# Kernel tuning notes

Measured on AMD Instinct MI355X. Metric: run time of the kernel, lower is better.

## Reference

```python
import jax, jax.numpy as jnp
import numpy as np

B, S, D, H = 4, 2048, 1024, 16
DH = D // H


def setup_inputs() -> dict:
    key = jax.random.key(0)
    ks = jax.random.split(key, 12)
    std = 0.02
    return {
        "inputs": jax.random.normal(ks[0], (B, S, D), jnp.float32),
        "pre_block": jax.random.normal(ks[1], (B, S, D), jnp.float32),
        "ln_gamma": jnp.ones((D,), jnp.float32),
        "ln_beta": jnp.zeros((D,), jnp.float32),
        "Wq": jax.random.normal(ks[2], (D, D), jnp.float32) * std,
        "bq": jnp.zeros((D,), jnp.float32),
        "Wk": jax.random.normal(ks[3], (D, D), jnp.float32) * std,
        "bk": jnp.zeros((D,), jnp.float32),
        "Wv": jax.random.normal(ks[4], (D, D), jnp.float32) * std,
        "bv": jnp.zeros((D,), jnp.float32),
        "Wpos": jax.random.normal(ks[5], (D, D), jnp.float32) * std,
        "u_bias": jax.random.normal(ks[6], (H, DH), jnp.float32) * std,
        "v_bias": jax.random.normal(ks[7], (H, DH), jnp.float32) * std,
        "Wo": jax.random.normal(ks[8], (D, D), jnp.float32) * std,
        "bo": jnp.zeros((D,), jnp.float32),
    }


def _sinusoidal_pe(seq_len, d_model, dtype):
    pos = jnp.arange(seq_len, dtype=dtype)[:, None]                 # [S,1]
    i = jnp.arange(0, d_model, 2, dtype=dtype)
    div = jnp.exp(-(jnp.log(jnp.asarray(10000.0, dtype)) * i / d_model))  # [D/2]
    ang = pos * div                                                  # [S,D/2]
    pe = jnp.zeros((seq_len, d_model), dtype)
    pe = pe.at[:, 0::2].set(jnp.sin(ang)).at[:, 1::2].set(jnp.cos(ang))
    return pe


def _rel_shift(pos_score):
    # Transformer-XL style relative shift: pos_score [B,H,S,S]
    b, h, s1, s2 = pos_score.shape
    pad = jnp.zeros((b, h, s1, 1), pos_score.dtype)
    padded = jnp.concatenate([pad, pos_score], axis=-1)              # [B,H,S,S+1]
    padded = padded.reshape(b, h, s2 + 1, s1)
    return padded[:, :, 1:].reshape(b, h, s1, s2)


def _layer_norm(x, gamma, beta, eps=1e-5):
    mu = jnp.mean(x, axis=-1, keepdims=True)
    var = jnp.mean(jnp.square(x - mu), axis=-1, keepdims=True)
    return (x - mu) * jax.lax.rsqrt(var + eps) * gamma + beta


def reference(inputs, pre_block, ln_gamma, ln_beta, Wq, bq, Wk, bk, Wv, bv,
              Wpos, u_bias, v_bias, Wo, bo):
    b, s, d = inputs.shape
    h = u_bias.shape[0]
    dh = d // h

    pe = _sinusoidal_pe(s, d, inputs.dtype)                          # [S,D]
    x = _layer_norm(inputs, ln_gamma, ln_beta)

    q = (x @ Wq + bq).reshape(b, s, h, dh)
    k = (x @ Wk + bk).reshape(b, s, h, dh)
    v = (pre_block @ Wv + bv).reshape(b, s, h, dh)
    p = (pe @ Wpos).reshape(s, h, dh)                                # shared across batch

    content = jnp.einsum('bshd,bthd->bhst', q + u_bias, k)           # [B,H,S,S]
    pos_score = jnp.einsum('bshd,thd->bhst', q + v_bias, p)          # [B,H,S,S]
    pos_score = _rel_shift(pos_score)

    score = (content + pos_score) / jnp.sqrt(jnp.asarray(d, inputs.dtype))
    attn = jax.nn.softmax(score, axis=-1)
    ctx = jnp.einsum('bhst,bthd->bshd', attn, v).reshape(b, s, d)
    return ctx @ Wo + bo
```

## Files before the change

kernel.cpp:

```cpp
#include <hip/hip_runtime.h>
#include <hip/hip_bf16.h>
#include <cmath>

#define B_ 4
#define S_ 2048
#define D_ 1024
#define H_ 16
#define DH_ 64

typedef __attribute__((ext_vector_type(8))) short short8;
typedef __attribute__((ext_vector_type(4))) float f32x4;
#define MFMA_BF16(a, b, c) __builtin_amdgcn_mfma_f32_16x16x32_bf16(a, b, c, 0, 0, 0)

static __device__ __forceinline__ float b2f(unsigned short u) {
  union { unsigned int i; float f; } x; x.i = ((unsigned int)u) << 16; return x.f;
}
static __device__ __forceinline__ unsigned short f2b(float f) {
  union { float f; unsigned int i; } x; x.f = f;
  unsigned int r = x.i + 0x7FFFu + ((x.i >> 16) & 1u);
  return (unsigned short)(r >> 16);
}
static __device__ __forceinline__ unsigned int pk2(float a, float b) {
  __hip_bfloat162 h = __float22bfloat162_rn(make_float2(a, b));
  return *(unsigned int*)&h;
}
static __device__ __forceinline__ int mod96(int x) {
  int t = x >> 5;
  int q = (t * 43691) >> 17;
  int m3 = t - q * 3;
  return (x & 31) + (m3 << 5);
}
static __device__ __forceinline__ int clampS(int x) {
  return x < 0 ? 0 : (x > S_ - 1 ? S_ - 1 : x);
}
typedef __attribute__((address_space(3))) unsigned int lds_u32_t;
typedef __attribute__((address_space(1))) const unsigned int glb_u32_t;
static __device__ __forceinline__ void gload_lds16(const void* g, void* l) {
  __builtin_amdgcn_global_load_lds((glb_u32_t*)g, (lds_u32_t*)l, 16, 0, 0);
}

__global__ __launch_bounds__(256) void prep_kernel(
    const float* __restrict__ inputs, const float* __restrict__ gamma,
    const float* __restrict__ beta, unsigned short* __restrict__ xb,
    const float* __restrict__ pre, unsigned short* __restrict__ preb,
    const double* __restrict__ dt, unsigned short* __restrict__ pe,
    const float* __restrict__ Wq, unsigned short* __restrict__ wtq,
    const float* __restrict__ Wk, unsigned short* __restrict__ wtk,
    const float* __restrict__ Wv, unsigned short* __restrict__ wtv,
    const float* __restrict__ Wp, unsigned short* __restrict__ wtp,
    const float* __restrict__ Wo, unsigned short* __restrict__ wto) {
  __shared__ __align__(16) float shf[64 * 65];
  int bid = blockIdx.x;
  int tid = threadIdx.x;
  if (bid < 8192) {
    int row = bid;
    float4 val = ((const float4*)(inputs + (size_t)row * D_))[tid];
    float s = val.x + val.y + val.z + val.w;
    float sq = val.x * val.x + val.y * val.y + val.z * val.z + val.w * val.w;
#pragma unroll
    for (int o = 32; o > 0; o >>= 1) {
      s += __shfl_down(s, o);
      sq += __shfl_down(sq, o);
    }
    int wid = tid >> 6;
    if ((tid & 63) == 0) { shf[wid] = s; shf[4 + wid] = sq; }
    __syncthreads();
    if (tid == 0) {
      float ts = shf[0] + shf[1] + shf[2] + shf[3];
      float tq = shf[4] + shf[5] + shf[6] + shf[7];
      float mu = ts * (1.0f / D_);
      float var = tq * (1.0f / D_) - mu * mu;
      shf[8] = mu;
      shf[9] = rsqrtf(var + 1e-5f);
    }
    __syncthreads();
    float mu = shf[8], rs = shf[9];
    float4 g = ((const float4*)gamma)[tid];
    float4 be = ((const float4*)beta)[tid];
    ushort4 o;
    o.x = f2b((val.x - mu) * rs * g.x + be.x);
    o.y = f2b((val.y - mu) * rs * g.y + be.y);
    o.z = f2b((val.z - mu) * rs * g.z + be.z);
    o.w = f2b((val.w - mu) * rs * g.w + be.w);
    *(ushort4*)(xb + (size_t)row * D_ + tid * 4) = o;
    return;
  }
  bid -= 8192;
  if (bid < 8192) {
    size_t idx = (size_t)(bid * 256 + tid) * 4;
    float4 v = *(const float4*)(pre + idx);
    ushort4 o; o.x = f2b(v.x); o.y = f2b(v.y); o.z = f2b(v.z); o.w = f2b(v.w);
    *(ushort4*)(preb + idx) = o;
    return;
  }
  bid -= 8192;
  if (bid < 4096) {
    int idx = bid * 256 + tid;
    int t = idx >> 9;
    int i = idx & 511;
    double ang = (double)t * dt[i];
    double k = floor(ang * 0.15915494309189535);
    float red = (float)(ang - k * 6.283185307179586);
    ushort2 sc;
    sc.x = f2b(sinf(red));
    sc.y = f2b(cosf(red));
    *(ushort2*)(pe + (size_t)t * D_ + 2 * i) = sc;
    return;
  }
  bid -= 4096;
  const float* W; unsigned short* WT;
  switch (bid >> 8) {
    case 0: W = Wq; WT = wtq; break;
    case 1: W = Wk; WT = wtk; break;
    case 2: W = Wv; WT = wtv; break;
    case 3: W = Wp; WT = wtp; break;
    default: W = Wo; WT = wto; break;
  }
  int tile = bid & 255;
  int n0 = (tile & 15) * 64, k0 = (tile >> 4) * 64;
#pragma unroll
  for (int c = 0; c < 4; c++) {
    int idx = tid + c * 256;
    int r = idx >> 4;
    int ch = (idx & 15) * 4;
    float4 d = *(const float4*)(W + (size_t)(k0 + r) * D_ + n0 + ch);
    shf[r * 65 + ch] = d.x; shf[r * 65 + ch + 1] = d.y;
    shf[r * 65 + ch + 2] = d.z; shf[r * 65 + ch + 3] = d.w;
  }
  __syncthreads();
  {
    int n = tid >> 2;
    int ch = (tid & 3) * 16;
    unsigned short tmp[8];
#pragma unroll
    for (int half = 0; half < 2; half++) {
#pragma unroll
      for (int e = 0; e < 8; e++) tmp[e] = f2b(shf[(ch + half * 8 + e) * 65 + n]);
      *(short8*)(WT + (size_t)(n0 + n) * D_ + k0 + ch + half * 8) = *(short8*)tmp;
    }
  }
}

template <bool F32OUT>
__global__ __launch_bounds__(256) void gemm_bf16_t(const unsigned short* __restrict__ A,
                                                   const unsigned short* __restrict__ BT,
                                                   const float* __restrict__ bias,
                                                   void* __restrict__ Cv,
                                                   int M, int N, int K) {
  __shared__ __align__(16) unsigned short As[128 * 32];
  __shared__ __align__(16) unsigned short Bs[128 * 32];
  const int tid = threadIdx.x;
  const int wid = tid >> 6, lane = tid & 63, quad = lane >> 4, l15 = lane & 15;
  const int m0 = blockIdx.y * 128, n0 = blockIdx.x * 128;
  const int moff = (wid >> 1) * 64, noff = (wid & 1) * 64;
  f32x4 acc[4][4];
#pragma unroll
  for (int i = 0; i < 4; i++)
#pragma unroll
    for (int j = 0; j < 4; j++) acc[i][j] = (f32x4){0.f, 0.f, 0.f, 0.f};

  const int cb0 = wid * 64;
  const int c0 = cb0 + lane;
  const int r0 = c0 >> 2, ch0 = (c0 & 3) * 8;
  const int c1 = c0 + 256;
  const int r1 = c1 >> 2, ch1 = (c1 & 3) * 8;

  for (int k0 = 0; k0 < K; k0 += 32) {
    __syncthreads();
    gload_lds16(A + (size_t)(m0 + r0) * K + k0 + ch0, &As[cb0 * 8]);
    gload_lds16(BT + (size_t)(n0 + r0) * K + k0 + ch0, &Bs[cb0 * 8]);
    gload_lds16(A + (size_t)(m0 + r1) * K + k0 + ch1, &As[(cb0 + 256) * 8]);
    gload_lds16(BT + (size_t)(n0 + r1) * K + k0 + ch1, &Bs[(cb0 + 256) * 8]);
    __syncthreads();
    short8 af[4], bf[4];
#pragma unroll
    for (int i = 0; i < 4; i++)
      af[i] = *(const short8*)&As[(moff + i * 16 + l15) * 32 + quad * 8];
#pragma unroll
    for (int j = 0; j < 4; j++)
      bf[j] = *(const short8*)&Bs[(noff + j * 16 + l15) * 32 + quad * 8];
#pragma unroll
    for (int i = 0; i < 4; i++)
#pragma unroll
      for (int j = 0; j < 4; j++) acc[i][j] = MFMA_BF16(af[i], bf[j], acc[i][j]);
  }
#pragma unroll
  for (int i = 0; i < 4; i++) {
    int row = m0 + moff + i * 16 + quad * 4;
#pragma unroll
    for (int j = 0; j < 4; j++) {
      int col = n0 + noff + j * 16 + l15;
      float bb = bias ? bias[col] : 0.f;
#pragma unroll
      for (int g = 0; g < 4; g++) {
        if (F32OUT)
          ((float*)Cv)[(size_t)(row + g) * N + col] = acc[i][j][g] + bb;
        else
          ((unsigned short*)Cv)[(size_t)(row + g) * N + col] = f2b(acc[i][j][g] + bb);
      }
    }
  }
}

__global__ __launch_bounds__(256) void gemm_qk_bf16(const unsigned short* __restrict__ A,
                                                    const unsigned short* __restrict__ BT,
                                                    const float* __restrict__ bq,
                                                    const float* __restrict__ bk,
                                                    unsigned short* __restrict__ outQ,
                                                    unsigned short* __restrict__ outK) {
  const int K = D_;
  __shared__ __align__(16) unsigned short As[128 * 32];
  __shared__ __align__(16) unsigned short Bs[128 * 32];
  const int tid = threadIdx.x;
  const int wid = tid >> 6, lane = tid & 63, quad = lane >> 4, l15 = lane & 15;
  const int m0 = blockIdx.y * 128, n0 = blockIdx.x * 128;
  const int moff = (wid >> 1) * 64, noff = (wid & 1) * 64;
  f32x4 acc[4][4];
#pragma unroll
  for (int i = 0; i < 4; i++)
#pragma unroll
    for (int j = 0; j < 4; j++) acc[i][j] = (f32x4){0.f, 0.f, 0.f, 0.f};

  const int cb0 = wid * 64;
  const int c0 = cb0 + lane;
  const int r0 = c0 >> 2, ch0 = (c0 & 3) * 8;
  const int c1 = c0 + 256;
  const int r1 = c1 >> 2, ch1 = (c1 & 3) * 8;

  for (int k0 = 0; k0 < K; k0 += 32) {
    __syncthreads();
    gload_lds16(A + (size_t)(m0 + r0) * K + k0 + ch0, &As[cb0 * 8]);
    gload_lds16(BT + (size_t)(n0 + r0) * K + k0 + ch0, &Bs[cb0 * 8]);
    gload_lds16(A + (size_t)(m0 + r1) * K + k0 + ch1, &As[(cb0 + 256) * 8]);
    gload_lds16(BT + (size_t)(n0 + r1) * K + k0 + ch1, &Bs[(cb0 + 256) * 8]);
    __syncthreads();
    short8 af[4], bf[4];
#pragma unroll
    for (int i = 0; i < 4; i++)
      af[i] = *(const short8*)&As[(moff + i * 16 + l15) * 32 + quad * 8];
#pragma unroll
    for (int j = 0; j < 4; j++)
      bf[j] = *(const short8*)&Bs[(noff + j * 16 + l15) * 32 + quad * 8];
#pragma unroll
    for (int i = 0; i < 4; i++)
#pragma unroll
      for (int j = 0; j < 4; j++) acc[i][j] = MFMA_BF16(af[i], bf[j], acc[i][j]);
  }
  const float* bias = (n0 < D_) ? bq : bk;
  unsigned short* outp = (n0 < D_) ? outQ : outK;
  const int nn0 = n0 & (D_ - 1);
#pragma unroll
  for (int i = 0; i < 4; i++) {
    int row = m0 + moff + i * 16 + quad * 4;
#pragma unroll
    for (int j = 0; j < 4; j++) {
      int col = nn0 + noff + j * 16 + l15;
      float bb = bias[col];
#pragma unroll
      for (int g = 0; g < 4; g++)
        outp[(size_t)(row + g) * D_ + col] = f2b(acc[i][j][g] + bb);
    }
  }
}

__global__ __launch_bounds__(256) void post_kernel(const unsigned short* __restrict__ v,
                                                   unsigned short* __restrict__ vt) {
  __shared__ __align__(16) unsigned short t[64 * 72];
  int bid = blockIdx.x;
  int tid = threadIdx.x;
  int s0 = (bid & 31) * 64, h = (bid >> 5) & 15, b = bid >> 9;
#pragma unroll
  for (int c = 0; c < 2; c++) {
    int idx = tid + c * 256;
    int r = idx >> 3, ch = (idx & 7) * 8;
    short8 d = *(const short8*)(v + (((size_t)b * S_ + s0 + r) * H_ + h) * DH_ + ch);
    *(short8*)&t[r * 72 + ch] = d;
  }
  __syncthreads();
  int dh = tid >> 2, ch = tid & 3;
  unsigned short tmp[8];
#pragma unroll
  for (int half = 0; half < 2; half++) {
#pragma unroll
    for (int e = 0; e < 8; e++) tmp[e] = t[(ch * 16 + half * 8 + e) * 72 + dh];
    *(short8*)(vt + ((size_t)(b * H_ + h) * 64 + dh) * S_ + s0 + ch * 16 + half * 8) =
        *(short8*)tmp;
  }
}

__global__ __launch_bounds__(256) void attn_kernel(const unsigned short* __restrict__ q,
                                                   const unsigned short* __restrict__ kg,
                                                   const unsigned short* __restrict__ vtg,
                                                   const unsigned short* __restrict__ pg,
                                                   const float* __restrict__ ub,
                                                   const float* __restrict__ vbias,
                                                   unsigned short* __restrict__ ctx) {
  int flat = blockIdx.x + 32 * (blockIdx.y + 16 * blockIdx.z);
  int swz = (flat & 7) * 256 + (flat >> 3);
  const int i0 = (swz & 31) * 64;
  const int h = (swz >> 5) & 15;
  const int b = swz >> 9;
  const int tid = threadIdx.x;
  const int wid = tid >> 6, lane = tid & 63, quad = lane >> 4, l15 = lane & 15;
  const int wr0 = wid * 16;
  const int ib = i0 >> 5;

  __shared__ __align__(16) unsigned short ks[32 * 64];
  __shared__ __align__(16) unsigned short ps[2][32 * 64];
  __shared__ __align__(16) unsigned short vts[2][64 * 32];
  __shared__ __align__(16) unsigned short prb[64 * 40];
  __shared__ __align__(16) unsigned short bandA[64 * 100];
  __shared__ __align__(16) unsigned short bandB[64 * 100];

  const int srow = tid >> 3;
  const int lcS = ((tid & 7) ^ (srow & 7)) * 8;
  const int vrow = tid >> 2, vch = (tid & 3) * 8;
  const int pc0 = (quad ^ (l15 & 7)) * 8;

  const unsigned short* kgl = kg + ((size_t)b * S_ * H_ + h) * DH_ + lcS;
  const unsigned short* pgl = pg + h * 64 + lcS;
  const unsigned short* vgl = vtg + ((size_t)(b * H_ + h) * 64 + vrow) * S_ + vch;
  const int wb = wid * 512;

  short8 qc0, qc1, qA0, qA1, qB0, qB1;
  {
    auto ldq2 = [&](int r, int c0, short8& outU, short8& outV) {
      int qi = i0 + r; if (qi > S_ - 1) qi = S_ - 1;
      short8 raw = *(const short8*)(q + (((size_t)b * S_ + qi) * H_ + h) * DH_ + c0);
      unsigned short tu[8], tv[8];
#pragma unroll
      for (int e = 0; e < 8; e++) {
        float f = b2f((unsigned short)raw[e]);
        tu[e] = f2b(f + ub[h * 64 + c0 + e]);
        tv[e] = f2b(f + vbias[h * 64 + c0 + e]);
      }
      outU = *(short8*)tu;
      outV = *(short8*)tv;
    };
    auto ldqv = [&](int r, int c0) -> short8 {
      int qi = i0 + r; if (qi > S_ - 1) qi = S_ - 1;
      short8 raw = *(const short8*)(q + (((size_t)b * S_ + qi) * H_ + h) * DH_ + c0);
      unsigned short tv[8];
#pragma unroll
      for (int e = 0; e < 8; e++)
        tv[e] = f2b(b2f((unsigned short)raw[e]) + vbias[h * 64 + c0 + e]);
      return *(short8*)tv;
    };
    ldq2(wr0 + l15, quad * 8, qc0, qA0);
    ldq2(wr0 + l15, 32 + quad * 8, qc1, qA1);
    qB0 = ldqv(wr0 + l15 + 1, quad * 8);
    qB1 = ldqv(wr0 + l15 + 1, 32 + quad * 8);
  }

  const int brow = (wr0 + l15) * 100;

  auto band_compute = [&](const unsigned short* src, int w, int rhi) {
    int rbase = rhi - 31;
    short8 a0 = w ? qB0 : qA0;
    short8 a1 = w ? qB1 : qA1;
    unsigned short* band = w ? bandB : bandA;
    const int OFF = w ? 2 : 1;
#pragma unroll
    for (int ct = 0; ct < 2; ct++) {
      int ro = (ct * 16 + l15) * 64;
      short8 b0 = *(const short8*)&src[ro + pc0];
      short8 b1 = *(const short8*)&src[ro + (pc0 ^ 32)];
      f32x4 acc = (f32x4){0.f, 0.f, 0.f, 0.f};
      acc = MFMA_BF16(b0, a0, acc);
      acc = MFMA_BF16(b1, a1, acc);
      int r0 = rbase + ct * 16 + quad * 4;
      int col = mod96(r0 + 960 + OFF);
      uint2 pv = make_uint2(pk2(acc[0], acc[1]), pk2(acc[2], acc[3]));
      *(uint2*)&band[brow + col] = pv;
      if (col == 0) *(uint2*)&band[brow + 96] = pv;
    }
  };

  {
    const int TW[5] = {0, 0, 0, 1, 1};
    const int TR[5] = {S_ + 30 - i0 - 64, S_ + 30 - i0 - 32, S_ + 30 - i0, 29, 61};
    {
      int rc = clampS(TR[0] - 31 + srow);
      gload_lds16(pgl + (size_t)rc * D_, &ps[0][wb]);
      gload_lds16(kgl + (size_t)srow * (H_ * DH_), &ks[wb]);
      gload_lds16(vgl, &vts[0][wb]);
    }
    __syncthreads();
#pragma unroll
    for (int t = 0; t < 5; t++) {
      if (t < 4) {
        int rc = clampS(TR[t + 1] - 31 + srow);
        gload_lds16(pgl + (size_t)rc * D_, &ps[(t + 1) & 1][wb]);
      }
      band_compute(ps[t & 1], TW[t], TR[t]);
      __syncthreads();
    }
  }

  float lsum = 0.f;
  f32x4 Oa[4];
#pragma unroll
  for (int ct = 0; ct < 4; ct++) Oa[ct] = (f32x4){0.f, 0.f, 0.f, 0.f};

  int cA = mod96(S_ + quad * 4 - i0 - wr0 - l15);
  int cB = mod96(2112 + quad * 4 - i0 - wr0 - l15);
  int cwin = 0, crhi = 0, chave = 0;

  const float SCL = 0.03125f;
  const unsigned int prbw = (wr0 + l15) * 40 + quad * 4;

  for (int jt = 0; jt < 64; jt++) {
    const int j0 = jt * 32;
    const int cur = jt & 1, nxt = cur ^ 1;
    int pwin = 0, prhi = 0, havep = 0;
    {
      int j0x = j0 + 32;
      if (j0x <= i0 + 63) { pwin = 0; prhi = S_ + 30 - i0 + j0x; havep = 1; }
      else if (jt < 63)   { pwin = 1; prhi = j0x - i0 + 29;      havep = 1; }
      if (havep) {
        int rc = clampS(prhi - 31 + srow);
        gload_lds16(pgl + (size_t)rc * D_, &ps[nxt][wb]);
      }
      if (jt < 63)
        gload_lds16(vgl + (size_t)(j0 + 32), &vts[nxt][wb]);
    }
    __builtin_amdgcn_s_setprio(1);
    if (chave) band_compute(ps[cur], cwin, crhi);
    f32x4 cc[2];
    {
#pragma unroll
      for (int ct = 0; ct < 2; ct++) {
        int ro = (ct * 16 + l15) * 64;
        short8 a0 = *(const short8*)&ks[ro + pc0];
        short8 a1 = *(const short8*)&ks[ro + (pc0 ^ 32)];
        f32x4 acc = (f32x4){0.f, 0.f, 0.f, 0.f};
        acc = MFMA_BF16(a0, qc0, acc);
        acc = MFMA_BF16(a1, qc1, acc);
        cc[ct] = acc;
      }
    }
    __builtin_amdgcn_s_setprio(0);
    __syncthreads();
    if (jt < 63)
      gload_lds16(kgl + (size_t)(j0 + 32 + srow) * (H_ * DH_), &ks[wb]);
    if (jt < ib) {
#pragma unroll
      for (int ct = 0; ct < 2; ct++) {
        int c0 = ct ? (cA + 16 >= 96 ? cA + 16 - 96 : cA + 16) : cA;
        const unsigned short* base = &bandA[brow + c0];
        float e0 = __expf((cc[ct][0] + b2f(base[0])) * SCL);
        float e1 = __expf((cc[ct][1] + b2f(base[1])) * SCL);
        float e2 = __expf((cc[ct][2] + b2f(base[2])) * SCL);
        float e3 = __expf((cc[ct][3] + b2f(base[3])) * SCL);
        *(uint2*)&prb[prbw + ct * 16] = make_uint2(pk2(e0, e1), pk2(e2, e3));
        lsum += (e0 + e1) + (e2 + e3);
      }
    } else if (jt >= ib + 3) {
#pragma unroll
      for (int ct = 0; ct < 2; ct++) {
        int c0 = ct ? (cB + 16 >= 96 ? cB + 16 - 96 : cB + 16) : cB;
        const unsigned short* base = &bandB[brow + c0];
        float e0 = __expf((cc[ct][0] + b2f(base[0])) * SCL);
        float e1 = __expf((cc[ct][1] + b2f(base[1])) * SCL);
        float e2 = __expf((cc[ct][2] + b2f(base[2])) * SCL);
        float e3 = __expf((cc[ct][3] + b2f(base[3])) * SCL);
        *(uint2*)&prb[prbw + ct * 16] = make_uint2(pk2(e0, e1), pk2(e2, e3));
        lsum += (e0 + e1) + (e2 + e3);
      }
    } else {
#pragma unroll
      for (int ct = 0; ct < 2; ct++) {
        int jbase = j0 + ct * 16 + quad * 4;
        float ev[4];
#pragma unroll
        for (int g = 0; g < 4; g++) {
          int d = jbase + g - (i0 + wr0 + l15);
          float t;
          if (d == 1) t = 0.f;
          else if (d <= 0) t = b2f(bandA[brow + mod96(S_ + d)]);
          else t = b2f(bandB[brow + mod96(d)]);
          ev[g] = __expf((cc[ct][g] + t) * SCL);
          lsum += ev[g];
        }
        *(uint2*)&prb[prbw + ct * 16] = make_uint2(pk2(ev[0], ev[1]), pk2(ev[2], ev[3]));
      }
    }
    {
      short8 af = *(const short8*)&prb[(wr0 + l15) * 40 + quad * 8];
#pragma unroll
      for (int ct = 0; ct < 4; ct++) {
        short8 bf = *(const short8*)&vts[cur][(ct * 16 + l15) * 32 + quad * 8];
        Oa[ct] = MFMA_BF16(af, bf, Oa[ct]);
      }
    }
    __syncthreads();
    cwin = pwin; crhi = prhi; chave = havep;
    cA += 32; if (cA >= 96) cA -= 96;
    cB += 32; if (cB >= 96) cB -= 96;
  }
  float ltot = lsum;
  ltot += __shfl_xor(ltot, 16);
  ltot += __shfl_xor(ltot, 32);
#pragma unroll
  for (int g = 0; g < 4; g++) {
    float lg = __shfl(ltot, quad * 4 + g);
    float inv = 1.f / lg;
    int i = i0 + wr0 + quad * 4 + g;
    unsigned short* dst = ctx + ((size_t)b * S_ + i) * D_ + h * 64;
#pragma unroll
    for (int ct = 0; ct < 4; ct++) dst[ct * 16 + l15] = f2b(Oa[ct][g] * inv);
  }
}

extern "C" void kernel_launch(void* const* d_in, const int* in_sizes, int n_in,
                              void* d_out, int out_size, void* d_ws, size_t ws_size,
                              hipStream_t stream) {
  const float* inputs = (const float*)d_in[0];
  const float* pre_block = (const float*)d_in[1];
  const float* ln_gamma = (const float*)d_in[2];
  const float* ln_beta = (const float*)d_in[3];
  const float* Wq = (const float*)d_in[4];
  const float* bq = (const float*)d_in[5];
  const float* Wk = (const float*)d_in[6];
  const float* bk = (const float*)d_in[7];
  const float* Wv = (const float*)d_in[8];
  const float* bv = (const float*)d_in[9];
  const float* Wpos = (const float*)d_in[10];
  const float* u_bias = (const float*)d_in[11];
  const float* v_bias = (const float*)d_in[12];
  const float* Wo = (const float*)d_in[13];
  const float* bo = (const float*)d_in[14];
  float* out = (float*)d_out;

  char* ws = (char*)d_ws;
  const size_t NBS = (size_t)B_ * S_ * D_;
  unsigned short* xb = (unsigned short*)ws;
  unsigned short* ctx = (unsigned short*)ws;
  unsigned short* preb = (unsigned short*)(ws + NBS * 2);
  unsigned short* peb = (unsigned short*)(ws + NBS * 4);
  char* base = ws + NBS * 4 + (size_t)S_ * D_ * 2;
  unsigned short* wtq = (unsigned short*)(base);
  unsigned short* wtk = (unsigned short*)(base + (size_t)D_ * D_ * 2);
  unsigned short* wtv = (unsigned short*)(base + (size_t)D_ * D_ * 4);
  unsigned short* wtp = (unsigned short*)(base + (size_t)D_ * D_ * 6);
  unsigned short* wto = (unsigned short*)(base + (size_t)D_ * D_ * 8);
  unsigned short* qb = (unsigned short*)(base + (size_t)D_ * D_ * 10);
  unsigned short* kb = qb + NBS;
  unsigned short* vb = kb + NBS;
  unsigned short* vtb = vb + NBS;
  unsigned short* pb = vtb + NBS;
  double* divtab = (double*)(pb + (size_t)S_ * D_);

  static double h_divtab[512];
  static bool h_init = false;
  if (!h_init) {
    for (int i = 0; i < 512; i++)
      h_divtab[i] = exp(-(log(10000.0) * (2.0 * i) / (double)D_));
    h_init = true;
  }
  hipMemcpyAsync(divtab, h_divtab, 512 * sizeof(double), hipMemcpyHostToDevice, stream);

  prep_kernel<<<21760, 256, 0, stream>>>(inputs, ln_gamma, ln_beta, xb,
                                         pre_block, preb, divtab, peb,
                                         Wq, wtq, Wk, wtk, Wv, wtv, Wpos, wtp, Wo, wto);
  gemm_qk_bf16<<<dim3(16, 64), 256, 0, stream>>>(xb, wtq, bq, bk, qb, kb);
  gemm_bf16_t<false><<<dim3(8, 64), 256, 0, stream>>>(preb, wtv, bv, vb, B_ * S_, D_, D_);
  gemm_bf16_t<false><<<dim3(8, 16), 256, 0, stream>>>(peb, wtp, nullptr, pb, S_, D_, D_);
  post_kernel<<<2048, 256, 0, stream>>>(vb, vtb);
  attn_kernel<<<dim3(32, 16, 4), 256, 0, stream>>>(qb, kb, vtb, pb, u_bias, v_bias, ctx);
  gemm_bf16_t<true><<<dim3(8, 64), 256, 0, stream>>>(ctx, wto, bo, out, B_ * S_, D_, D_);
}
```

Measured before the change: 614.6 us.

## Fuse Q/K/V/pos GEMMs into one launch with transposed V epilogue; rework attention prefetch

Merges the QK, V and positional projection GEMMs into a single grouped kernel dispatched by block index. The V epilogue writes the transposed layout directly, which removes the separate transpose kernel and the intermediate V buffer. In the attention loop, K is now double-buffered and V single-buffered, with the V load issued at the top of the iteration, a mid-loop barrier dropped and an explicit vmcnt wait added. This cuts launch count and memory round-trips, but the new load ordering relies on vmcnt counting that could be fragile.

Result: faster. 575.7 us (-6.3%).

```diff
diff --git a/kernel.cpp b/kernel.cpp
--- a/kernel.cpp
+++ b/kernel.cpp
@@ -141,73 +141,11 @@
   }
 }
 
-template <bool F32OUT>
-__global__ __launch_bounds__(256) void gemm_bf16_t(const unsigned short* __restrict__ A,
-                                                   const unsigned short* __restrict__ BT,
-                                                   const float* __restrict__ bias,
-                                                   void* __restrict__ Cv,
-                                                   int M, int N, int K) {
-  __shared__ __align__(16) unsigned short As[128 * 32];
-  __shared__ __align__(16) unsigned short Bs[128 * 32];
-  const int tid = threadIdx.x;
-  const int wid = tid >> 6, lane = tid & 63, quad = lane >> 4, l15 = lane & 15;
-  const int m0 = blockIdx.y * 128, n0 = blockIdx.x * 128;
-  const int moff = (wid >> 1) * 64, noff = (wid & 1) * 64;
-  f32x4 acc[4][4];
-#pragma unroll
-  for (int i = 0; i < 4; i++)
-#pragma unroll
-    for (int j = 0; j < 4; j++) acc[i][j] = (f32x4){0.f, 0.f, 0.f, 0.f};
-
-  const int cb0 = wid * 64;
-  const int c0 = cb0 + lane;
-  const int r0 = c0 >> 2, ch0 = (c0 & 3) * 8;
-  const int c1 = c0 + 256;
-  const int r1 = c1 >> 2, ch1 = (c1 & 3) * 8;
-
-  for (int k0 = 0; k0 < K; k0 += 32) {
-    __syncthreads();
-    gload_lds16(A + (size_t)(m0 + r0) * K + k0 + ch0, &As[cb0 * 8]);
-    gload_lds16(BT + (size_t)(n0 + r0) * K + k0 + ch0, &Bs[cb0 * 8]);
-    gload_lds16(A + (size_t)(m0 + r1) * K + k0 + ch1, &As[(cb0 + 256) * 8]);
-    gload_lds16(BT + (size_t)(n0 + r1) * K + k0 + ch1, &Bs[(cb0 + 256) * 8]);
-    __syncthreads();
-    short8 af[4], bf[4];
-#pragma unroll
-    for (int i = 0; i < 4; i++)
-      af[i] = *(const short8*)&As[(moff + i * 16 + l15) * 32 + quad * 8];
-#pragma unroll
-    for (int j = 0; j < 4; j++)
-      bf[j] = *(const short8*)&Bs[(noff + j * 16 + l15) * 32 + quad * 8];
-#pragma unroll
-    for (int i = 0; i < 4; i++)
-#pragma unroll
-      for (int j = 0; j < 4; j++) acc[i][j] = MFMA_BF16(af[i], bf[j], acc[i][j]);
-  }
-#pragma unroll
-  for (int i = 0; i < 4; i++) {
-    int row = m0 + moff + i * 16 + quad * 4;
-#pragma unroll
-    for (int j = 0; j < 4; j++) {
-      int col = n0 + noff + j * 16 + l15;
-      float bb = bias ? bias[col] : 0.f;
-#pragma unroll
-      for (int g = 0; g < 4; g++) {
-        if (F32OUT)
-          ((float*)Cv)[(size_t)(row + g) * N + col] = acc[i][j][g] + bb;
-        else
-          ((unsigned short*)Cv)[(size_t)(row + g) * N + col] = f2b(acc[i][j][g] + bb);
-      }
-    }
-  }
-}
-
-__global__ __launch_bounds__(256) void gemm_qk_bf16(const unsigned short* __restrict__ A,
+__global__ __launch_bounds__(256) void gemm_out_f32(const unsigned short* __restrict__ A,
                                                     const unsigned short* __restrict__ BT,
-                                                    const float* __restrict__ bq,
-                                                    const float* __restrict__ bk,
-                                                    unsigned short* __restrict__ outQ,
-                                                    unsigned short* __restrict__ outK) {
+                                                    const float* __restrict__ bias,
+                                                    float* __restrict__ C,
+                                                    int N) {
   const int K = D_;
   __shared__ __align__(16) unsigned short As[128 * 32];
   __shared__ __align__(16) unsigned short Bs[128 * 32];
@@ -246,45 +184,124 @@
 #pragma unroll
       for (int j = 0; j < 4; j++) acc[i][j] = MFMA_BF16(af[i], bf[j], acc[i][j]);
   }
-  const float* bias = (n0 < D_) ? bq : bk;
-  unsigned short* outp = (n0 < D_) ? outQ : outK;
-  const int nn0 = n0 & (D_ - 1);
 #pragma unroll
   for (int i = 0; i < 4; i++) {
     int row = m0 + moff + i * 16 + quad * 4;
 #pragma unroll
     for (int j = 0; j < 4; j++) {
-      int col = nn0 + noff + j * 16 + l15;
+      int col = n0 + noff + j * 16 + l15;
       float bb = bias[col];
 #pragma unroll
       for (int g = 0; g < 4; g++)
-        outp[(size_t)(row + g) * D_ + col] = f2b(acc[i][j][g] + bb);
-    }
-  }
-}
-
-__global__ __launch_bounds__(256) void post_kernel(const unsigned short* __restrict__ v,
-                                                   unsigned short* __restrict__ vt) {
-  __shared__ __align__(16) unsigned short t[64 * 72];
+        C[(size_t)(row + g) * N + col] = acc[i][j][g] + bb;
+    }
+  }
+}
+
+__global__ __launch_bounds__(256) void gemm_fused(
+    const unsigned short* __restrict__ xb, const unsigned short* __restrict__ preb,
+    const unsigned short* __restrict__ peb, const unsigned short* __restrict__ wtqk,
+    const unsigned short* __restrict__ wtv, const unsigned short* __restrict__ wtp,
+    const float* __restrict__ bq, const float* __restrict__ bk,
+    const float* __restrict__ bv, unsigned short* __restrict__ outQ,
+    unsigned short* __restrict__ outK, unsigned short* __restrict__ vtb,
+    unsigned short* __restrict__ outP) {
+  const int K = D_;
+  __shared__ __align__(16) unsigned short As[128 * 32];
+  __shared__ __align__(16) unsigned short Bs[128 * 32];
   int bid = blockIdx.x;
-  int tid = threadIdx.x;
-  int s0 = (bid & 31) * 64, h = (bid >> 5) & 15, b = bid >> 9;
-#pragma unroll
-  for (int c = 0; c < 2; c++) {
-    int idx = tid + c * 256;
-    int r = idx >> 3, ch = (idx & 7) * 8;
-    short8 d = *(const short8*)(v + (((size_t)b * S_ + s0 + r) * H_ + h) * DH_ + ch);
-    *(short8*)&t[r * 72 + ch] = d;
-  }
-  __syncthreads();
-  int dh = tid >> 2, ch = tid & 3;
-  unsigned short tmp[8];
-#pragma unroll
-  for (int half = 0; half < 2; half++) {
-#pragma unroll
-    for (int e = 0; e < 8; e++) tmp[e] = t[(ch * 16 + half * 8 + e) * 72 + dh];
-    *(short8*)(vt + ((size_t)(b * H_ + h) * 64 + dh) * S_ + s0 + ch * 16 + half * 8) =
-        *(short8*)tmp;
+  const unsigned short *A, *BT;
+  int m0, n0, mode;
+  if (bid < 1024) {
+    mode = 0; A = xb; BT = wtqk;
+    n0 = (bid & 15) * 128; m0 = (bid >> 4) * 128;
+  } else if (bid < 1536) {
+    int i = bid - 1024; mode = 1; A = preb; BT = wtv;
+    n0 = (i & 7) * 128; m0 = (i >> 3) * 128;
+  } else {
+    int i = bid - 1536; mode = 2; A = peb; BT = wtp;
+    n0 = (i & 7) * 128; m0 = (i >> 3) * 128;
+  }
+  const int tid = threadIdx.x;
+  const int wid = tid >> 6, lane = tid & 63, quad = lane >> 4, l15 = lane & 15;
+  const int moff = (wid >> 1) * 64, noff = (wid & 1) * 64;
+  f32x4 acc[4][4];
+#pragma unroll
+  for (int i = 0; i < 4; i++)
+#pragma unroll
+    for (int j = 0; j < 4; j++) acc[i][j] = (f32x4){0.f, 0.f, 0.f, 0.f};
+
+  const int cb0 = wid * 64;
+  const int c0 = cb0 + lane;
+  const int r0 = c0 >> 2, ch0 = (c0 & 3) * 8;
+  const int c1 = c0 + 256;
+  const int r1 = c1 >> 2, ch1 = (c1 & 3) * 8;
+
+  for (int k0 = 0; k0 < K; k0 += 32) {
+    __syncthreads();
+    gload_lds16(A + (size_t)(m0 + r0) * K + k0 + ch0, &As[cb0 * 8]);
+    gload_lds16(BT + (size_t)(n0 + r0) * K + k0 + ch0, &Bs[cb0 * 8]);
+    gload_lds16(A + (size_t)(m0 + r1) * K + k0 + ch1, &As[(cb0 + 256) * 8]);
+    gload_lds16(BT + (size_t)(n0 + r1) * K + k0 + ch1, &Bs[(cb0 + 256) * 8]);
+    __syncthreads();
+    short8 af[4], bf[4];
+#pragma unroll
+    for (int i = 0; i < 4; i++)
+      af[i] = *(const short8*)&As[(moff + i * 16 + l15) * 32 + quad * 8];
+#pragma unroll
+    for (int j = 0; j < 4; j++)
+      bf[j] = *(const short8*)&Bs[(noff + j * 16 + l15) * 32 + quad * 8];
+#pragma unroll
+    for (int i = 0; i < 4; i++)
+#pragma unroll
+      for (int j = 0; j < 4; j++) acc[i][j] = MFMA_BF16(af[i], bf[j], acc[i][j]);
+  }
+
+  if (mode == 0) {
+    const float* bias = (n0 < D_) ? bq : bk;
+    unsigned short* outp = (n0 < D_) ? outQ : outK;
+    const int nn0 = n0 & (D_ - 1);
+#pragma unroll
+    for (int i = 0; i < 4; i++) {
+      int row = m0 + moff + i * 16 + quad * 4;
+#pragma unroll
+      for (int j = 0; j < 4; j++) {
+        int col = nn0 + noff + j * 16 + l15;
+        float bb = bias[col];
+#pragma unroll
+        for (int g = 0; g < 4; g++)
+          outp[(size_t)(row + g) * D_ + col] = f2b(acc[i][j][g] + bb);
+      }
+    }
+  } else if (mode == 1) {
+#pragma unroll
+    for (int i = 0; i < 4; i++) {
+      int row = m0 + moff + i * 16 + quad * 4;
+      int bb_ = row >> 11, s = row & (S_ - 1);
+#pragma unroll
+      for (int j = 0; j < 4; j++) {
+        int col = n0 + noff + j * 16 + l15;
+        float bias = bv[col];
+        ushort4 o;
+        o.x = f2b(acc[i][j][0] + bias);
+        o.y = f2b(acc[i][j][1] + bias);
+        o.z = f2b(acc[i][j][2] + bias);
+        o.w = f2b(acc[i][j][3] + bias);
+        *(ushort4*)(vtb + ((size_t)(bb_ * 1024 + col)) * S_ + s) = o;
+      }
+    }
+  } else {
+#pragma unroll
+    for (int i = 0; i < 4; i++) {
+      int row = m0 + moff + i * 16 + quad * 4;
+#pragma unroll
+      for (int j = 0; j < 4; j++) {
+        int col = n0 + noff + j * 16 + l15;
+#pragma unroll
+        for (int g = 0; g < 4; g++)
+          outP[(size_t)(row + g) * D_ + col] = f2b(acc[i][j][g]);
+      }
+    }
   }
 }
 
@@ -305,9 +322,9 @@
   const int wr0 = wid * 16;
   const int ib = i0 >> 5;
 
-  __shared__ __align__(16) unsigned short ks[32 * 64];
+  __shared__ __align__(16) unsigned short ks[2][32 * 64];
   __shared__ __align__(16) unsigned short ps[2][32 * 64];
-  __shared__ __align__(16) unsigned short vts[2][64 * 32];
+  __shared__ __align__(16) unsigned short vts[64 * 32];
   __shared__ __align__(16) unsigned short prb[64 * 40];
   __shared__ __align__(16) unsigned short bandA[64 * 100];
   __shared__ __align__(16) unsigned short bandB[64 * 100];
@@ -382,8 +399,7 @@
     {
       int rc = clampS(TR[0] - 31 + srow);
       gload_lds16(pgl + (size_t)rc * D_, &ps[0][wb]);
-      gload_lds16(kgl + (size_t)srow * (H_ * DH_), &ks[wb]);
-      gload_lds16(vgl, &vts[0][wb]);
+      gload_lds16(kgl + (size_t)srow * (H_ * DH_), &ks[0][wb]);
     }
     __syncthreads();
 #pragma unroll
@@ -412,17 +428,16 @@
   for (int jt = 0; jt < 64; jt++) {
     const int j0 = jt * 32;
     const int cur = jt & 1, nxt = cur ^ 1;
-    int pwin = 0, prhi = 0, havep = 0;
+    int nwin, nrhi;
     {
+      gload_lds16(vgl + (size_t)j0, &vts[wb]);
+      int j0n = (jt < 63) ? j0 + 32 : j0;
+      gload_lds16(kgl + (size_t)(j0n + srow) * (H_ * DH_), &ks[nxt][wb]);
       int j0x = j0 + 32;
-      if (j0x <= i0 + 63) { pwin = 0; prhi = S_ + 30 - i0 + j0x; havep = 1; }
-      else if (jt < 63)   { pwin = 1; prhi = j0x - i0 + 29;      havep = 1; }
-      if (havep) {
-        int rc = clampS(prhi - 31 + srow);
-        gload_lds16(pgl + (size_t)rc * D_, &ps[nxt][wb]);
-      }
-      if (jt < 63)
-        gload_lds16(vgl + (size_t)(j0 + 32), &vts[nxt][wb]);
+      if (j0x <= i0 + 63) { nwin = 0; nrhi = S_ + 30 - i0 + j0x; }
+      else                { nwin = 1; nrhi = j0x - i0 + 29; }
+      int rc = clampS(nrhi - 31 + srow);
+      gload_lds16(pgl + (size_t)rc * D_, &ps[nxt][wb]);
     }
     __builtin_amdgcn_s_setprio(1);
     if (chave) band_compute(ps[cur], cwin, crhi);
@@ -431,8 +446,8 @@
 #pragma unroll
       for (int ct = 0; ct < 2; ct++) {
         int ro = (ct * 16 + l15) * 64;
-        short8 a0 = *(const short8*)&ks[ro + pc0];
-        short8 a1 = *(const short8*)&ks[ro + (pc0 ^ 32)];
+        short8 a0 = *(const short8*)&ks[cur][ro + pc0];
+        short8 a1 = *(const short8*)&ks[cur][ro + (pc0 ^ 32)];
         f32x4 acc = (f32x4){0.f, 0.f, 0.f, 0.f};
         acc = MFMA_BF16(a0, qc0, acc);
         acc = MFMA_BF16(a1, qc1, acc);
@@ -440,9 +455,6 @@
       }
     }
     __builtin_amdgcn_s_setprio(0);
-    __syncthreads();
-    if (jt < 63)
-      gload_lds16(kgl + (size_t)(j0 + 32 + srow) * (H_ * DH_), &ks[wb]);
     if (jt < ib) {
 #pragma unroll
       for (int ct = 0; ct < 2; ct++) {
@@ -485,16 +497,17 @@
         *(uint2*)&prb[prbw + ct * 16] = make_uint2(pk2(ev[0], ev[1]), pk2(ev[2], ev[3]));
       }
     }
+    asm volatile("s_waitcnt vmcnt(2)" ::: "memory");
     {
       short8 af = *(const short8*)&prb[(wr0 + l15) * 40 + quad * 8];
 #pragma unroll
       for (int ct = 0; ct < 4; ct++) {
-        short8 bf = *(const short8*)&vts[cur][(ct * 16 + l15) * 32 + quad * 8];
+        short8 bf = *(const short8*)&vts[(ct * 16 + l15) * 32 + quad * 8];
         Oa[ct] = MFMA_BF16(af, bf, Oa[ct]);
       }
     }
     __syncthreads();
-    cwin = pwin; crhi = prhi; chave = havep;
+    cwin = nwin; crhi = nrhi; chave = 1;
     cA += 32; if (cA >= 96) cA -= 96;
     cB += 32; if (cB >= 96) cB -= 96;
   }
@@ -546,8 +559,7 @@
   unsigned short* wto = (unsigned short*)(base + (size_t)D_ * D_ * 8);
   unsigned short* qb = (unsigned short*)(base + (size_t)D_ * D_ * 10);
   unsigned short* kb = qb + NBS;
-  unsigned short* vb = kb + NBS;
-  unsigned short* vtb = vb + NBS;
+  unsigned short* vtb = kb + NBS;
   unsigned short* pb = vtb + NBS;
   double* divtab = (double*)(pb + (size_t)S_ * D_);
 
@@ -563,10 +575,8 @@
   prep_kernel<<<21760, 256, 0, stream>>>(inputs, ln_gamma, ln_beta, xb,
                                          pre_block, preb, divtab, peb,
                                          Wq, wtq, Wk, wtk, Wv, wtv, Wpos, wtp, Wo, wto);
-  gemm_qk_bf16<<<dim3(16, 64), 256, 0, stream>>>(xb, wtq, bq, bk, qb, kb);
-  gemm_bf16_t<false><<<dim3(8, 64), 256, 0, stream>>>(preb, wtv, bv, vb, B_ * S_, D_, D_);
-  gemm_bf16_t<false><<<dim3(8, 16), 256, 0, stream>>>(peb, wtp, nullptr, pb, S_, D_, D_);
-  post_kernel<<<2048, 256, 0, stream>>>(vb, vtb);
+  gemm_fused<<<1664, 256, 0, stream>>>(xb, preb, peb, wtq, wtv, wtp,
+                                       bq, bk, bv, qb, kb, vtb, pb);
   attn_kernel<<<dim3(32, 16, 4), 256, 0, stream>>>(qb, kb, vtb, pb, u_bias, v_bias, ctx);
-  gemm_bf16_t<true><<<dim3(8, 64), 256, 0, stream>>>(ctx, wto, bo, out, B_ * S_, D_, D_);
-}
+  gemm_out_f32<<<dim3(8, 64), 256, 0, stream>>>(ctx, wto, bo, out, D_);
+}
```
